# Performance work log

Measured on AMD Instinct MI355X. Metric: run time of the kernel, lower is better.

## Reference

```python
import jax, jax.numpy as jnp
import numpy as np

INPUTDIM = 256
OUTDIM = 256
GRIDSIZE = 300


def setup_inputs() -> dict:
    key = jax.random.key(0)
    k1, k2 = jax.random.split(key)
    x = jax.random.normal(k1, (1024, INPUTDIM), dtype=jnp.float32)
    scale = 1.0 / (np.sqrt(INPUTDIM) * np.sqrt(GRIDSIZE))
    fouriercoeffs = jax.random.normal(k2, (2, OUTDIM, INPUTDIM, GRIDSIZE), dtype=jnp.float32) * scale
    bias = jnp.zeros((1, OUTDIM), dtype=jnp.float32)
    return {"x": x, "fouriercoeffs": fouriercoeffs, "bias": bias}


def reference(x, fouriercoeffs, bias):
    # x: (B, I); fouriercoeffs: (2, O, I, G); bias: (1, O)
    outshape = x.shape[:-1] + (OUTDIM,)
    xf = x.reshape(-1, INPUTDIM)
    k = jnp.arange(1, GRIDSIZE + 1, dtype=xf.dtype)  # (G,)
    phase = xf[:, :, None] * k[None, None, :]        # (B, I, G)
    c = jnp.cos(phase)
    s = jnp.sin(phase)
    y = jnp.einsum('big,jig->bj', c, fouriercoeffs[0]) \
        + jnp.einsum('big,jig->bj', s, fouriercoeffs[1])
    y = y + bias
    return y.reshape(outshape)
```

## Files before the change

kernel.cpp:

```cpp
#include <hip/hip_runtime.h>

#define BATCH   1024
#define IDIM    256
#define ODIM    256
#define GRIDSZ  300
#define KS_     64
#define IPW     4
#define CHUNKS  19
#define NSTEPS  (IPW * CHUNKS)
#define INV2PI  0.15915494309189535f

typedef __attribute__((ext_vector_type(8))) short  short8;
typedef __attribute__((ext_vector_type(4))) float  f32x4;
typedef __attribute__((ext_vector_type(4))) unsigned int u32x4;

__device__ __forceinline__ unsigned pk(float c, float s) {
  unsigned a = __float_as_uint(c) + 0x8000u;
  unsigned b = __float_as_uint(s) + 0x8000u;
  return __builtin_amdgcn_perm(b, a, 0x07060302u);
}

__device__ __forceinline__ void dma16(const float* g, const float* l) {
  __builtin_amdgcn_global_load_lds(
      (const __attribute__((address_space(1))) unsigned int*)(g),
      (__attribute__((address_space(3))) unsigned int*)(l), 16, 0, 0);
}

__device__ __forceinline__ void rot(float& c, float& s, float C, float S) {
  float t1 = s * S, t2 = c * S;
  float cn = __builtin_fmaf(c, C, -t1);
  s = __builtin_fmaf(s, C, t2);
  c = cn;
}

__device__ __forceinline__ void cossin(float rev, float& c, float& s) {
  c = __builtin_amdgcn_cosf(__builtin_amdgcn_fractf(rev));
  s = __builtin_amdgcn_cosf(__builtin_amdgcn_fractf(rev - 0.25f));
}

__global__ void init_out(const float* __restrict__ bias, float* __restrict__ out) {
  const int idx = blockIdx.x * 256 + threadIdx.x;
  out[idx] = bias[idx & (ODIM - 1)];
}

__global__ __launch_bounds__(256, 4) void fkan_pipe(
    const float* __restrict__ x, const float* __restrict__ fc,
    float* __restrict__ out) {
  __shared__ alignas(16) unsigned int Bp[2][1024];
  __shared__ alignas(16) float Bf[2][2048];

  const int tid = threadIdx.x, id = blockIdx.x;
  const int z = id & 7;
  const int m = (id >> 3) & 3;
  const int nk = (id >> 5) * 8 + z;
  const int n  = nk & 3;
  const int ks = nk >> 2;

  const int wave = tid >> 6, lane = tid & 63;
  const int fr = lane & 15, fq = lane >> 4;
  const int mbase = m * 256 + wave * 64;
  const int nbase = n * 64;

  f32x4 acc[4][4];
#pragma unroll
  for (int a_ = 0; a_ < 4; ++a_)
#pragma unroll
    for (int b_ = 0; b_ < 4; ++b_)
      acc[a_][b_] = (f32x4){0.f, 0.f, 0.f, 0.f};

  float r1c[4], r1s[4], r16c[4], r16s[4], sc_[4], ss_[4];

  const float* b1 = fc + (size_t)ODIM * IDIM * GRIDSZ;

  int fo = ((nbase + wave * 16 + fr) * IDIM + ks * IPW) * GRIDSZ + fq * 4;
  const int sa = wave * 256 + lane * 4;

  dma16(fc + fo, &Bf[0][sa]);
  dma16(b1 + fo, &Bf[0][1024 + sa]);
  fo += 16;
  dma16(fc + fo, &Bf[1][sa]);
  dma16(b1 + fo, &Bf[1][1024 + sa]);

  asm volatile("s_waitcnt vmcnt(2)" ::: "memory");
  {
    const f32x4 La = *(const f32x4*)&Bf[0][sa];
    const f32x4 Lb = *(const f32x4*)&Bf[0][1024 + sa];
    *(u32x4*)&Bp[0][sa] =
        (u32x4){pk(La.x, Lb.x), pk(La.y, Lb.y), pk(La.z, Lb.z), pk(La.w, Lb.w)};
  }

  int gs = 0, il = 0;
  int gd = 2;
  bool zpA = false;

#pragma unroll 2
  for (int S = 0; S < NSTEPS; ++S) {
    __builtin_amdgcn_sched_barrier(0);
    asm volatile("s_waitcnt lgkmcnt(0)" ::: "memory");
    __builtin_amdgcn_s_barrier();
    __builtin_amdgcn_sched_barrier(0);

    if (gs == 0) {
      const int i = ks * IPW + il;
#pragma unroll
      for (int tI = 0; tI < 4; ++tI) {
        const float xr = x[(size_t)(mbase + tI * 16 + fr) * IDIM + i] * INV2PI;
        cossin(xr, r1c[tI], r1s[tI]);
        cossin(16.0f * xr, r16c[tI], r16s[tI]);
        cossin((float)(fq * 4 + 1) * xr, sc_[tI], ss_[tI]);
      }
    }

    bool zpB = false;
    if (S < NSTEPS - 2) {
      if (gd == 0) fo += GRIDSZ - (CHUNKS - 1) * 16;
      else fo += 16;
      zpB = (gd == CHUNKS - 1) & (fq == 3);
      const int sub = zpB ? 4 : 0;
      dma16(fc + fo - sub, &Bf[S & 1][sa]);
      dma16(b1 + fo - sub, &Bf[S & 1][1024 + sa]);
      gd++; if (gd == CHUNKS) gd = 0;
    }

    const unsigned int* buf = &Bp[S & 1][0];
    short8 bV0 = __builtin_bit_cast(short8, *(const u32x4*)(buf + lane * 4));
    short8 bV1 = __builtin_bit_cast(short8, *(const u32x4*)(buf + 256 + lane * 4));
    short8 bV2 = __builtin_bit_cast(short8, *(const u32x4*)(buf + 512 + lane * 4));
    short8 bV3 = __builtin_bit_cast(short8, *(const u32x4*)(buf + 768 + lane * 4));

#pragma unroll
    for (int tI = 0; tI < 4; ++tI) {
      float c = sc_[tI], s = ss_[tI];
      unsigned a0 = pk(c, s);
      rot(c, s, r1c[tI], r1s[tI]); unsigned a1 = pk(c, s);
      rot(c, s, r1c[tI], r1s[tI]); unsigned a2 = pk(c, s);
      rot(c, s, r1c[tI], r1s[tI]); unsigned a3 = pk(c, s);
      rot(sc_[tI], ss_[tI], r16c[tI], r16s[tI]);
      short8 aV = __builtin_bit_cast(short8, (u32x4){a0, a1, a2, a3});
      acc[tI][0] = __builtin_amdgcn_mfma_f32_16x16x32_bf16(aV, bV0, acc[tI][0], 0, 0, 0);
      acc[tI][1] = __builtin_amdgcn_mfma_f32_16x16x32_bf16(aV, bV1, acc[tI][1], 0, 0, 0);
      acc[tI][2] = __builtin_amdgcn_mfma_f32_16x16x32_bf16(aV, bV2, acc[tI][2], 0, 0, 0);
      acc[tI][3] = __builtin_amdgcn_mfma_f32_16x16x32_bf16(aV, bV3, acc[tI][3], 0, 0, 0);
    }

    if (S < NSTEPS - 1) {
      if (S < NSTEPS - 2) {
        asm volatile("s_waitcnt vmcnt(2)" ::: "memory");
      } else {
        asm volatile("s_waitcnt vmcnt(0)" ::: "memory");
      }
      const f32x4 La = *(const f32x4*)&Bf[(S + 1) & 1][sa];
      const f32x4 Lb = *(const f32x4*)&Bf[(S + 1) & 1][1024 + sa];
      u32x4 w = (u32x4){pk(La.x, Lb.x), pk(La.y, Lb.y),
                        pk(La.z, Lb.z), pk(La.w, Lb.w)};
      if (zpA) w = (u32x4){0u, 0u, 0u, 0u};
      *(u32x4*)&Bp[(S + 1) & 1][sa] = w;
    }
    zpA = zpB;
    gs++; if (gs == CHUNKS) { gs = 0; ++il; }
  }

  const int ob = mbase + fq * 4;
  const int oj = nbase + fr;
#pragma unroll
  for (int tI = 0; tI < 4; ++tI)
#pragma unroll
    for (int tJ = 0; tJ < 4; ++tJ) {
      float* dst = out + (size_t)(ob + tI * 16) * ODIM + (oj + tJ * 16);
#pragma unroll
      for (int rr = 0; rr < 4; ++rr)
        unsafeAtomicAdd(dst + rr * ODIM, acc[tI][tJ][rr]);
    }
}

extern "C" void kernel_launch(void* const* d_in, const int* in_sizes, int n_in,
                              void* d_out, int out_size, void* d_ws, size_t ws_size,
                              hipStream_t stream) {
  const float* x    = (const float*)d_in[0];
  const float* fc   = (const float*)d_in[1];
  const float* bias = (const float*)d_in[2];
  float* out = (float*)d_out;

  init_out<<<dim3(BATCH * ODIM / 256), dim3(256), 0, stream>>>(bias, out);
  fkan_pipe<<<dim3(4 * 4 * KS_), dim3(256), 0, stream>>>(x, fc, out);
}
```

Baseline: 322.2 us.

## Replace split-K atomic accumulation with workspace partials and a reduction kernel

Each split-K block now writes its partial output tile with plain stores into a per-slice workspace, and a separate reduction kernel sums the 64 slices and adds the bias. This removes the fp32 atomic adds and their contention on the output. In exchange it writes and reads back 64 MB of partials (64 slices × 1024×256 floats). The old atomic path remains as a fallback when the workspace is too small.

```diff
diff --git a/kernel.cpp b/kernel.cpp
--- a/kernel.cpp
+++ b/kernel.cpp
@@ -43,6 +43,23 @@
   out[idx] = bias[idx & (ODIM - 1)];
 }
 
+__global__ __launch_bounds__(256) void reduce_ws(
+    const float* __restrict__ ws, const float* __restrict__ bias,
+    float* __restrict__ out) {
+  const int t = blockIdx.x * 256 + threadIdx.x;
+  const int base = t * 4;
+  f32x4 s = (f32x4){0.f, 0.f, 0.f, 0.f};
+#pragma unroll 8
+  for (int k = 0; k < KS_; ++k) {
+    const f32x4 v = *(const f32x4*)(ws + (size_t)k * (BATCH * ODIM) + base);
+    s.x += v.x; s.y += v.y; s.z += v.z; s.w += v.w;
+  }
+  const f32x4 bv = *(const f32x4*)(bias + (base & (ODIM - 1)));
+  s.x += bv.x; s.y += bv.y; s.z += bv.z; s.w += bv.w;
+  *(f32x4*)(out + base) = s;
+}
+
+template <int TPL>
 __global__ __launch_bounds__(256, 4) void fkan_pipe(
     const float* __restrict__ x, const float* __restrict__ fc,
     float* __restrict__ out) {
@@ -162,15 +179,28 @@
 
   const int ob = mbase + fq * 4;
   const int oj = nbase + fr;
-#pragma unroll
-  for (int tI = 0; tI < 4; ++tI)
-#pragma unroll
-    for (int tJ = 0; tJ < 4; ++tJ) {
-      float* dst = out + (size_t)(ob + tI * 16) * ODIM + (oj + tJ * 16);
-#pragma unroll
-      for (int rr = 0; rr < 4; ++rr)
-        unsafeAtomicAdd(dst + rr * ODIM, acc[tI][tJ][rr]);
-    }
+  if (TPL) {
+    float* wsl = out + (size_t)ks * (BATCH * ODIM);
+#pragma unroll
+    for (int tI = 0; tI < 4; ++tI)
+#pragma unroll
+      for (int tJ = 0; tJ < 4; ++tJ) {
+        float* dst = wsl + (size_t)(ob + tI * 16) * ODIM + (oj + tJ * 16);
+#pragma unroll
+        for (int rr = 0; rr < 4; ++rr)
+          dst[rr * ODIM] = acc[tI][tJ][rr];
+      }
+  } else {
+#pragma unroll
+    for (int tI = 0; tI < 4; ++tI)
+#pragma unroll
+      for (int tJ = 0; tJ < 4; ++tJ) {
+        float* dst = out + (size_t)(ob + tI * 16) * ODIM + (oj + tJ * 16);
+#pragma unroll
+        for (int rr = 0; rr < 4; ++rr)
+          unsafeAtomicAdd(dst + rr * ODIM, acc[tI][tJ][rr]);
+      }
+  }
 }
 
 extern "C" void kernel_launch(void* const* d_in, const int* in_sizes, int n_in,
@@ -181,6 +211,13 @@
   const float* bias = (const float*)d_in[2];
   float* out = (float*)d_out;
 
-  init_out<<<dim3(BATCH * ODIM / 256), dim3(256), 0, stream>>>(bias, out);
-  fkan_pipe<<<dim3(4 * 4 * KS_), dim3(256), 0, stream>>>(x, fc, out);
-}
+  const size_t need = (size_t)KS_ * BATCH * ODIM * 4;
+  if (ws_size >= need) {
+    float* ws = (float*)d_ws;
+    fkan_pipe<1><<<dim3(4 * 4 * KS_), dim3(256), 0, stream>>>(x, fc, ws);
+    reduce_ws<<<dim3(BATCH * ODIM / 1024), dim3(256), 0, stream>>>(ws, bias, out);
+  } else {
+    init_out<<<dim3(BATCH * ODIM / 256), dim3(256), 0, stream>>>(bias, out);
+    fkan_pipe<0><<<dim3(4 * 4 * KS_), dim3(256), 0, stream>>>(x, fc, out);
+  }
+}
```

New measurement: 321.5 us. About the same (-0.2%).
